# Kernel optimization log

Hardware: AMD Instinct MI355X
Metric: run time of the kernel (lower is better)

The kernel has to match this reference:

```python
import jax, jax.numpy as jnp
import numpy as np

B, T, HID = 64, 512, 8192
C = 64            # num_channels (graph nodes)
NH = 4            # attention heads
HD = 16           # head_dim = graph_dim // num_heads
GD = 64           # graph_dim
IN_DIM = 128      # input_dim = channel_dim


def setup_inputs() -> dict:
    key = jax.random.key(0)
    ks = jax.random.split(key, 7)
    return {
        "H": jax.random.normal(ks[0], (B, T, HID), jnp.float32),
        "W_embed": jax.random.normal(ks[1], (GD, IN_DIM), jnp.float32) * 0.05,
        "b_embed": jax.random.normal(ks[2], (GD,), jnp.float32) * 0.05,
        "Wh_w": jax.random.normal(ks[3], (NH, HD, GD), jnp.float32) * 0.1,
        "a_w": jax.random.normal(ks[4], (NH, 2 * HD), jnp.float32) * 0.1,
        "Wr": jax.random.normal(ks[5], (IN_DIM, GD), jnp.float32) * 0.1,
        "br": jax.random.normal(ks[6], (IN_DIM,), jnp.float32) * 0.05,
    }


def reference(H, W_embed, b_embed, Wh_w, a_w, Wr, br):
    b, t, hid = H.shape
    ch = hid // C  # = IN_DIM
    # channel-wise temporal mean pooling -> graph node inputs [B, C, ch]
    node_inputs = H.reshape(b, t, C, ch).mean(axis=1)
    # node embedding [B, C, GD]
    nodes = jnp.einsum('bcf,gf->bcg', node_inputs, W_embed) + b_embed
    # per-head projection [B, NH, C, HD]
    Wh = jnp.einsum('bcg,hog->bhco', nodes, Wh_w)
    # split concat-score: cat([Wh_i, Wh_j]) @ a == (Wh@a1)_i + (Wh@a2)_j
    s1 = jnp.einsum('bhco,ho->bhc', Wh, a_w[:, :HD])
    s2 = jnp.einsum('bhco,ho->bhc', Wh, a_w[:, HD:])
    e = jax.nn.leaky_relu(s1[:, :, :, None] + s2[:, :, None, :], 0.2)  # [B,NH,C,C]
    attn = jax.nn.softmax(e, axis=-1)
    head_out = jax.nn.elu(jnp.einsum('bhij,bhjo->bhio', attn, Wh))  # [B,NH,C,HD]
    # concat heads along feature dim -> [B, C, GD]
    n_prime = head_out.transpose(0, 2, 1, 3).reshape(b, C, NH * HD)
    # readout on node-mean
    g = jax.nn.relu(jnp.einsum('bg,ig->bi', n_prime.mean(axis=1), Wr) + br)
    return g, attn
```

## Files before the change

kernel.cpp:

```cpp
#include <hip/hip_runtime.h>
#include <math.h>

#define NB 64
#define NT 512
#define HID 8192
#define NC 64
#define NH 4
#define HD 16
#define GD 64
#define IN_DIM 128
#define TSPLIT 4

typedef float f32x4 __attribute__((ext_vector_type(4)));

__global__ __launch_bounds__(1024) void pool_kernel(const float* __restrict__ H,
                                                    float* __restrict__ part,
                                                    int ts_count) {
    const int ts = blockIdx.x;
    const int b = blockIdx.y;
    const int tid = threadIdx.x;
    const int rows = NT / ts_count;
    const f32x4* src = reinterpret_cast<const f32x4*>(H + (size_t)b * NT * HID) +
                       (size_t)(ts * rows) * (HID / 4);
    f32x4 a0 = (f32x4)0.f;
    f32x4 a1 = (f32x4)0.f;
#pragma unroll 4
    for (int t = 0; t < rows; ++t) {
        f32x4 v0 = __builtin_nontemporal_load(&src[(size_t)t * (HID / 4) + tid]);
        f32x4 v1 = __builtin_nontemporal_load(&src[(size_t)t * (HID / 4) + tid + 1024]);
        a0 += v0;
        a1 += v1;
    }
    f32x4* dst = reinterpret_cast<f32x4*>(part + ((size_t)ts * NB + b) * HID);
    dst[tid] = a0;
    dst[tid + 1024] = a1;
}

#define SNI 132
#define SP  68

#define OFF_NI    0
#define OFF_NODES 0
#define OFF_HO    0
#define OFF_WRT   0
#define OFF_WH    4352
#define OFF_WE    8704
#define OFF_WW    8704
#define OFF_S1    8704
#define OFF_S2    8960
#define OFF_PM    9216
#define OFF_PS    10240
#define OFF_M     11264
#define OFF_INV   11520
#define OFF_MEAN  11776
#define SMEM_FLOATS 13056

__global__ __launch_bounds__(1024) void tail_kernel(
    const float* __restrict__ part,
    const float* __restrict__ W_embed,
    const float* __restrict__ b_embed,
    const float* __restrict__ Wh_w,
    const float* __restrict__ a_w,
    const float* __restrict__ Wr,
    const float* __restrict__ br,
    float* __restrict__ out_g,
    float* __restrict__ out_attn,
    int ts_count)
{
    __shared__ float smem[SMEM_FLOATS];
    const int tid = threadIdx.x;
    const int b = blockIdx.x;

#pragma unroll
    for (int k = 0; k < 2; ++k) {
        int idx4 = tid + k * 1024;
        int c = idx4 >> 5, f4 = (idx4 & 31) << 2;
        f32x4 s = (f32x4)0.f;
        for (int ts = 0; ts < ts_count; ++ts)
            s += reinterpret_cast<const f32x4*>(part + ((size_t)ts * NB + b) * HID)[idx4];
        *reinterpret_cast<f32x4*>(&smem[OFF_NI + c * SNI + f4]) = s * (1.0f / NT);
    }
#pragma unroll
    for (int k = 0; k < 4; ++k) {
        int idx = tid + k * 1024;
        int g = idx >> 6, f = idx & 63;
        smem[OFF_WE + f * SP + g] = W_embed[g * IN_DIM + f];
    }
    __syncthreads();

    const int c_g = tid >> 4;
    const int g4 = (tid & 15) << 2;
    f32x4 acc1 = *reinterpret_cast<const f32x4*>(&b_embed[g4]);
#pragma unroll 8
    for (int f = 0; f < 64; ++f) {
        float n = smem[OFF_NI + c_g * SNI + f];
        f32x4 w = *reinterpret_cast<const f32x4*>(&smem[OFF_WE + f * SP + g4]);
        acc1 += n * w;
    }
    __syncthreads();
#pragma unroll
    for (int k = 0; k < 4; ++k) {
        int idx = tid + k * 1024;
        int g = idx >> 6, f = idx & 63;
        smem[OFF_WE + f * SP + g] = W_embed[g * IN_DIM + 64 + f];
    }
    __syncthreads();
#pragma unroll 8
    for (int f = 0; f < 64; ++f) {
        float n = smem[OFF_NI + c_g * SNI + 64 + f];
        f32x4 w = *reinterpret_cast<const f32x4*>(&smem[OFF_WE + f * SP + g4]);
        acc1 += n * w;
    }
    __syncthreads();

    *reinterpret_cast<f32x4*>(&smem[OFF_NODES + c_g * SP + g4]) = acc1;
#pragma unroll
    for (int k = 0; k < 4; ++k) {
        int idx = tid + k * 1024;
        int ho = idx >> 6, g = idx & 63;
        smem[OFF_WW + g * SP + ho] = Wh_w[ho * GD + g];
    }
    __syncthreads();

    f32x4 acc2 = (f32x4)0.f;
#pragma unroll 8
    for (int g = 0; g < GD; ++g) {
        float n = smem[OFF_NODES + c_g * SP + g];
        f32x4 w = *reinterpret_cast<const f32x4*>(&smem[OFF_WW + g * SP + g4]);
        acc2 += n * w;
    }
    *reinterpret_cast<f32x4*>(&smem[OFF_WH + c_g * SP + g4]) = acc2;
    __syncthreads();

    if (tid < 256) {
        int c = tid >> 2, h = tid & 3;
        float a1 = 0.f, a2 = 0.f;
#pragma unroll
        for (int o = 0; o < HD; ++o) {
            float w = smem[OFF_WH + c * SP + h * HD + o];
            a1 += w * a_w[h * 2 * HD + o];
            a2 += w * a_w[h * 2 * HD + HD + o];
        }
        smem[OFF_S1 + h * NC + c] = a1;
        smem[OFF_S2 + h * NC + c] = a2;
    }
    __syncthreads();

    {
        const int r = tid & 255, q = tid >> 8;
        const int i = r & 63, h = r >> 6;
        const float s1 = smem[OFF_S1 + h * NC + i];
        float pm = -1e30f;
#pragma unroll
        for (int jj = 0; jj < 16; ++jj) {
            float x = s1 + smem[OFF_S2 + h * NC + q * 16 + jj];
            float e = x > 0.f ? x : 0.2f * x;
            pm = fmaxf(pm, e);
        }
        smem[OFF_PM + q * 256 + r] = pm;
        __syncthreads();
        const float m = fmaxf(fmaxf(smem[OFF_PM + r], smem[OFF_PM + 256 + r]),
                              fmaxf(smem[OFF_PM + 512 + r], smem[OFF_PM + 768 + r]));
        float ps = 0.f;
#pragma unroll
        for (int jj = 0; jj < 16; ++jj) {
            float x = s1 + smem[OFF_S2 + h * NC + q * 16 + jj];
            float e = x > 0.f ? x : 0.2f * x;
            ps += __expf(e - m);
        }
        smem[OFF_PS + q * 256 + r] = ps;
        __syncthreads();
        if (tid < 256) {
            smem[OFF_M + tid] = m;
            smem[OFF_INV + tid] = 1.0f / (smem[OFF_PS + tid] + smem[OFF_PS + 256 + tid] +
                                          smem[OFF_PS + 512 + tid] + smem[OFF_PS + 768 + tid]);
        }
    }
    __syncthreads();

    f32x4* attn_b = reinterpret_cast<f32x4*>(out_attn + (size_t)b * NH * NC * NC);
#pragma unroll
    for (int k = 0; k < 4; ++k) {
        int idx4 = tid + k * 1024;
        int h = idx4 >> 10, i = (idx4 >> 4) & 63, j = (idx4 & 15) << 2;
        int r = h * 64 + i;
        float s1 = smem[OFF_S1 + h * NC + i];
        float m = smem[OFF_M + r], inv = smem[OFF_INV + r];
        f32x4 p;
        {
            float x = s1 + smem[OFF_S2 + h * NC + j + 0];
            float e = x > 0.f ? x : 0.2f * x; p.x = __expf(e - m) * inv;
        }
        {
            float x = s1 + smem[OFF_S2 + h * NC + j + 1];
            float e = x > 0.f ? x : 0.2f * x; p.y = __expf(e - m) * inv;
        }
        {
            float x = s1 + smem[OFF_S2 + h * NC + j + 2];
            float e = x > 0.f ? x : 0.2f * x; p.z = __expf(e - m) * inv;
        }
        {
            float x = s1 + smem[OFF_S2 + h * NC + j + 3];
            float e = x > 0.f ? x : 0.2f * x; p.w = __expf(e - m) * inv;
        }
        attn_b[idx4] = p;
    }

    {
        const int og = tid & 3, i = (tid >> 2) & 63, h = tid >> 8;
        const int r = h * 64 + i;
        const float s1 = smem[OFF_S1 + h * NC + i];
        const float m = smem[OFF_M + r], inv = smem[OFF_INV + r];
        f32x4 a = (f32x4)0.f;
        for (int j = 0; j < NC; ++j) {
            float x = s1 + smem[OFF_S2 + h * NC + j];
            float e = x > 0.f ? x : 0.2f * x;
            float p = __expf(e - m) * inv;
            f32x4 w = *reinterpret_cast<const f32x4*>(
                &smem[OFF_WH + j * SP + h * HD + og * 4]);
            a += p * w;
        }
        f32x4 o;
        o.x = a.x > 0.f ? a.x : expm1f(a.x);
        o.y = a.y > 0.f ? a.y : expm1f(a.y);
        o.z = a.z > 0.f ? a.z : expm1f(a.z);
        o.w = a.w > 0.f ? a.w : expm1f(a.w);
        *reinterpret_cast<f32x4*>(&smem[OFF_HO + i * SP + h * HD + og * 4]) = o;
    }
    __syncthreads();

    if (tid < 256) {
        int g = tid & 63, q = tid >> 6;
        float s = 0.f;
#pragma unroll
        for (int ii = 0; ii < 16; ++ii)
            s += smem[OFF_HO + (q * 16 + ii) * SP + g];
        smem[OFF_PM + q * 64 + g] = s;
    }
    __syncthreads();
    if (tid < 64)
        smem[OFF_MEAN + tid] = (smem[OFF_PM + tid] + smem[OFF_PM + 64 + tid] +
                                smem[OFF_PM + 128 + tid] + smem[OFF_PM + 192 + tid]) *
                               (1.0f / NC);
    __syncthreads();

#pragma unroll
    for (int k = 0; k < 8; ++k) {
        int idx = tid + k * 1024;
        int io = idx >> 6, g = idx & 63;
        smem[OFF_WRT + g * 132 + io] = Wr[io * GD + g];
    }
    __syncthreads();
    if (tid < IN_DIM) {
        float acc = br[tid];
#pragma unroll 8
        for (int g = 0; g < GD; ++g)
            acc += smem[OFF_MEAN + g] * smem[OFF_WRT + g * 132 + tid];
        out_g[(size_t)b * IN_DIM + tid] = fmaxf(acc, 0.f);
    }
}

extern "C" void kernel_launch(void* const* d_in, const int* in_sizes, int n_in,
                              void* d_out, int out_size, void* d_ws, size_t ws_size,
                              hipStream_t stream) {
    const float* H       = (const float*)d_in[0];
    const float* W_embed = (const float*)d_in[1];
    const float* b_embed = (const float*)d_in[2];
    const float* Wh_w    = (const float*)d_in[3];
    const float* a_w     = (const float*)d_in[4];
    const float* Wr      = (const float*)d_in[5];
    const float* br      = (const float*)d_in[6];
    float* out = (float*)d_out;
    float* out_attn = out + NB * IN_DIM;

    const size_t need4 = (size_t)TSPLIT * NB * HID * sizeof(float);
    const int ts = (ws_size >= need4) ? TSPLIT : 1;
    float* part = (float*)d_ws;

    pool_kernel<<<dim3(ts, NB), dim3(1024), 0, stream>>>(H, part, ts);
    tail_kernel<<<dim3(NB), dim3(1024), 0, stream>>>(
        part, W_embed, b_embed, Wh_w, a_w, Wr, br, out, out_attn, ts);
}
```

Before: 189.1 us.

## Fuse pooling and tail into one kernel with last-block atomic handoff

```diff
diff --git a/kernel.cpp b/kernel.cpp
--- a/kernel.cpp
+++ b/kernel.cpp
@@ -13,32 +13,8 @@
 
 typedef float f32x4 __attribute__((ext_vector_type(4)));
 
-__global__ __launch_bounds__(1024) void pool_kernel(const float* __restrict__ H,
-                                                    float* __restrict__ part,
-                                                    int ts_count) {
-    const int ts = blockIdx.x;
-    const int b = blockIdx.y;
-    const int tid = threadIdx.x;
-    const int rows = NT / ts_count;
-    const f32x4* src = reinterpret_cast<const f32x4*>(H + (size_t)b * NT * HID) +
-                       (size_t)(ts * rows) * (HID / 4);
-    f32x4 a0 = (f32x4)0.f;
-    f32x4 a1 = (f32x4)0.f;
-#pragma unroll 4
-    for (int t = 0; t < rows; ++t) {
-        f32x4 v0 = __builtin_nontemporal_load(&src[(size_t)t * (HID / 4) + tid]);
-        f32x4 v1 = __builtin_nontemporal_load(&src[(size_t)t * (HID / 4) + tid + 1024]);
-        a0 += v0;
-        a1 += v1;
-    }
-    f32x4* dst = reinterpret_cast<f32x4*>(part + ((size_t)ts * NB + b) * HID);
-    dst[tid] = a0;
-    dst[tid + 1024] = a1;
-}
-
 #define SNI 132
 #define SP  68
-
 #define OFF_NI    0
 #define OFF_NODES 0
 #define OFF_HO    0
@@ -55,8 +31,10 @@
 #define OFF_MEAN  11776
 #define SMEM_FLOATS 13056
 
-__global__ __launch_bounds__(1024) void tail_kernel(
-    const float* __restrict__ part,
+__global__ __launch_bounds__(1024) void fused_kernel(
+    const float* __restrict__ H,
+    float* __restrict__ part,
+    unsigned* __restrict__ cnt,
     const float* __restrict__ W_embed,
     const float* __restrict__ b_embed,
     const float* __restrict__ Wh_w,
@@ -68,16 +46,44 @@
     int ts_count)
 {
     __shared__ float smem[SMEM_FLOATS];
+    __shared__ unsigned sm_last;
     const int tid = threadIdx.x;
-    const int b = blockIdx.x;
+    const int ts = blockIdx.x;
+    const int b = blockIdx.y;
+
+    {
+        const int rows = NT / ts_count;
+        const f32x4* src = reinterpret_cast<const f32x4*>(H + (size_t)b * NT * HID) +
+                           (size_t)(ts * rows) * (HID / 4);
+        f32x4 a0 = (f32x4)0.f;
+        f32x4 a1 = (f32x4)0.f;
+#pragma unroll 4
+        for (int t = 0; t < rows; ++t) {
+            f32x4 v0 = __builtin_nontemporal_load(&src[(size_t)t * (HID / 4) + tid]);
+            f32x4 v1 = __builtin_nontemporal_load(&src[(size_t)t * (HID / 4) + tid + 1024]);
+            a0 += v0;
+            a1 += v1;
+        }
+        f32x4* dst = reinterpret_cast<f32x4*>(part + ((size_t)ts * NB + b) * HID);
+        dst[tid] = a0;
+        dst[tid + 1024] = a1;
+    }
+    __syncthreads();
+    if (tid == 0) {
+        unsigned prev = __hip_atomic_fetch_add(&cnt[b], 1u, __ATOMIC_ACQ_REL,
+                                               __HIP_MEMORY_SCOPE_AGENT);
+        sm_last = (prev == (unsigned)(ts_count - 1)) ? 1u : 0u;
+    }
+    __syncthreads();
+    if (!sm_last) return;
 
 #pragma unroll
     for (int k = 0; k < 2; ++k) {
         int idx4 = tid + k * 1024;
         int c = idx4 >> 5, f4 = (idx4 & 31) << 2;
         f32x4 s = (f32x4)0.f;
-        for (int ts = 0; ts < ts_count; ++ts)
-            s += reinterpret_cast<const f32x4*>(part + ((size_t)ts * NB + b) * HID)[idx4];
+        for (int t = 0; t < ts_count; ++t)
+            s += reinterpret_cast<const f32x4*>(part + ((size_t)t * NB + b) * HID)[idx4];
         *reinterpret_cast<f32x4*>(&smem[OFF_NI + c * SNI + f4]) = s * (1.0f / NT);
     }
 #pragma unroll
@@ -88,14 +94,20 @@
     }
     __syncthreads();
 
-    const int c_g = tid >> 4;
-    const int g4 = (tid & 15) << 2;
-    f32x4 acc1 = *reinterpret_cast<const f32x4*>(&b_embed[g4]);
-#pragma unroll 8
-    for (int f = 0; f < 64; ++f) {
-        float n = smem[OFF_NI + c_g * SNI + f];
-        f32x4 w = *reinterpret_cast<const f32x4*>(&smem[OFF_WE + f * SP + g4]);
-        acc1 += n * w;
+    const int rq = (tid & 255) >> 4;
+    const int q4 = (tid & 15) << 2;
+    f32x4 acc[4];
+    if (tid < 256) {
+        f32x4 bias = *reinterpret_cast<const f32x4*>(&b_embed[q4]);
+#pragma unroll
+        for (int cc = 0; cc < 4; ++cc) acc[cc] = bias;
+#pragma unroll 4
+        for (int f = 0; f < 64; ++f) {
+            f32x4 w = *reinterpret_cast<const f32x4*>(&smem[OFF_WE + f * SP + q4]);
+#pragma unroll
+            for (int cc = 0; cc < 4; ++cc)
+                acc[cc] += smem[OFF_NI + (rq * 4 + cc) * SNI + f] * w;
+        }
     }
     __syncthreads();
 #pragma unroll
@@ -105,15 +117,22 @@
         smem[OFF_WE + f * SP + g] = W_embed[g * IN_DIM + 64 + f];
     }
     __syncthreads();
-#pragma unroll 8
-    for (int f = 0; f < 64; ++f) {
-        float n = smem[OFF_NI + c_g * SNI + 64 + f];
-        f32x4 w = *reinterpret_cast<const f32x4*>(&smem[OFF_WE + f * SP + g4]);
-        acc1 += n * w;
-    }
-    __syncthreads();
-
-    *reinterpret_cast<f32x4*>(&smem[OFF_NODES + c_g * SP + g4]) = acc1;
+    if (tid < 256) {
+#pragma unroll 4
+        for (int f = 0; f < 64; ++f) {
+            f32x4 w = *reinterpret_cast<const f32x4*>(&smem[OFF_WE + f * SP + q4]);
+#pragma unroll
+            for (int cc = 0; cc < 4; ++cc)
+                acc[cc] += smem[OFF_NI + (rq * 4 + cc) * SNI + 64 + f] * w;
+        }
+    }
+    __syncthreads();
+
+    if (tid < 256) {
+#pragma unroll
+        for (int cc = 0; cc < 4; ++cc)
+            *reinterpret_cast<f32x4*>(&smem[OFF_NODES + (rq * 4 + cc) * SP + q4]) = acc[cc];
+    }
 #pragma unroll
     for (int k = 0; k < 4; ++k) {
         int idx = tid + k * 1024;
@@ -122,27 +141,34 @@
     }
     __syncthreads();
 
-    f32x4 acc2 = (f32x4)0.f;
-#pragma unroll 8
-    for (int g = 0; g < GD; ++g) {
-        float n = smem[OFF_NODES + c_g * SP + g];
-        f32x4 w = *reinterpret_cast<const f32x4*>(&smem[OFF_WW + g * SP + g4]);
-        acc2 += n * w;
-    }
-    *reinterpret_cast<f32x4*>(&smem[OFF_WH + c_g * SP + g4]) = acc2;
+    if (tid < 256) {
+        f32x4 a2[4];
+#pragma unroll
+        for (int cc = 0; cc < 4; ++cc) a2[cc] = (f32x4)0.f;
+#pragma unroll 4
+        for (int g = 0; g < GD; ++g) {
+            f32x4 w = *reinterpret_cast<const f32x4*>(&smem[OFF_WW + g * SP + q4]);
+#pragma unroll
+            for (int cc = 0; cc < 4; ++cc)
+                a2[cc] += smem[OFF_NODES + (rq * 4 + cc) * SP + g] * w;
+        }
+#pragma unroll
+        for (int cc = 0; cc < 4; ++cc)
+            *reinterpret_cast<f32x4*>(&smem[OFF_WH + (rq * 4 + cc) * SP + q4]) = a2[cc];
+    }
     __syncthreads();
 
     if (tid < 256) {
         int c = tid >> 2, h = tid & 3;
-        float a1 = 0.f, a2 = 0.f;
+        float a1 = 0.f, a2s = 0.f;
 #pragma unroll
         for (int o = 0; o < HD; ++o) {
             float w = smem[OFF_WH + c * SP + h * HD + o];
             a1 += w * a_w[h * 2 * HD + o];
-            a2 += w * a_w[h * 2 * HD + HD + o];
+            a2s += w * a_w[h * 2 * HD + HD + o];
         }
         smem[OFF_S1 + h * NC + c] = a1;
-        smem[OFF_S2 + h * NC + c] = a2;
+        smem[OFF_S2 + h * NC + c] = a2s;
     }
     __syncthreads();
 
@@ -252,11 +278,11 @@
     }
     __syncthreads();
     if (tid < IN_DIM) {
-        float acc = br[tid];
+        float accv = br[tid];
 #pragma unroll 8
         for (int g = 0; g < GD; ++g)
-            acc += smem[OFF_MEAN + g] * smem[OFF_WRT + g * 132 + tid];
-        out_g[(size_t)b * IN_DIM + tid] = fmaxf(acc, 0.f);
+            accv += smem[OFF_MEAN + g] * smem[OFF_WRT + g * 132 + tid];
+        out_g[(size_t)b * IN_DIM + tid] = fmaxf(accv, 0.f);
     }
 }
 
@@ -273,11 +299,12 @@
     float* out = (float*)d_out;
     float* out_attn = out + NB * IN_DIM;
 
-    const size_t need4 = (size_t)TSPLIT * NB * HID * sizeof(float);
+    const size_t need4 = (size_t)TSPLIT * NB * HID * sizeof(float) + NB * sizeof(unsigned);
     const int ts = (ws_size >= need4) ? TSPLIT : 1;
     float* part = (float*)d_ws;
-
-    pool_kernel<<<dim3(ts, NB), dim3(1024), 0, stream>>>(H, part, ts);
-    tail_kernel<<<dim3(NB), dim3(1024), 0, stream>>>(
-        part, W_embed, b_embed, Wh_w, a_w, Wr, br, out, out_attn, ts);
+    unsigned* cnt = (unsigned*)(part + (size_t)ts * NB * HID);
+
+    hipMemsetAsync(cnt, 0, NB * sizeof(unsigned), stream);
+    fused_kernel<<<dim3(ts, NB), dim3(1024), 0, stream>>>(
+        H, part, cnt, W_embed, b_embed, Wh_w, a_w, Wr, br, out, out_attn, ts);
 }
```

Result: slower. 202.3 us (+7.0%).
